# Performance work log

Measured on AMD Instinct MI355X. Metric: run time of the kernel, lower is better.

## Reference

```python
import jax, jax.numpy as jnp
import numpy as np

B, T, N, D = 8, 12, 325, 256
H = 8
HD = D // H
FF = 1024
SCALE = HD ** -0.5
EPS = 1e-5
NEG_INF = jnp.float32(-1e30)


def layernorm(x, w, b):
    mu = jnp.mean(x, axis=-1, keepdims=True)
    var = jnp.mean(jnp.square(x - mu), axis=-1, keepdims=True)
    return (x - mu) * jax.lax.rsqrt(var + EPS) * w + b


def mha(x, wq, bq, wk, bk, wv, bv, wo, bo, mask):
    # x: (G, L, D); mask: (L, L) bool, True = keep, or None
    G, L, _ = x.shape
    q = (x @ wq + bq).reshape(G, L, H, HD)
    k = (x @ wk + bk).reshape(G, L, H, HD)
    v = (x @ wv + bv).reshape(G, L, H, HD)
    scores = jnp.einsum('glhd,gmhd->ghlm', q, k) * SCALE
    if mask is not None:
        scores = jnp.where(mask[None, None], scores, NEG_INF)
    attn = jax.nn.softmax(scores, axis=-1)
    out = jnp.einsum('ghlm,gmhd->glhd', attn, v).reshape(G, L, D)
    return out @ wo + bo


def setup_inputs() -> dict:
    key = jax.random.key(0)
    ks = jax.random.split(key, 16)
    s = 0.02
    inp = {
        'x': jax.random.normal(ks[0], (B, T, N, D), jnp.float32),
        'adj_mask': jax.random.randint(ks[1], (N, N), 0, 2, jnp.int32),
        'sa_wq': jax.random.normal(ks[2], (D, D)) * s, 'sa_bq': jnp.zeros((D,)),
        'sa_wk': jax.random.normal(ks[3], (D, D)) * s, 'sa_bk': jnp.zeros((D,)),
        'sa_wv': jax.random.normal(ks[4], (D, D)) * s, 'sa_bv': jnp.zeros((D,)),
        'sa_wo': jax.random.normal(ks[5], (D, D)) * s, 'sa_bo': jnp.zeros((D,)),
        'sa_ln_w': jnp.ones((D,)), 'sa_ln_b': jnp.zeros((D,)),
        'ta_wq': jax.random.normal(ks[6], (D, D)) * s, 'ta_bq': jnp.zeros((D,)),
        'ta_wk': jax.random.normal(ks[7], (D, D)) * s, 'ta_bk': jnp.zeros((D,)),
        'ta_wv': jax.random.normal(ks[8], (D, D)) * s, 'ta_bv': jnp.zeros((D,)),
        'ta_wo': jax.random.normal(ks[9], (D, D)) * s, 'ta_bo': jnp.zeros((D,)),
        'ta_ln_w': jnp.ones((D,)), 'ta_ln_b': jnp.zeros((D,)),
        'f_w1': jax.random.normal(ks[10], (D, FF)) * s, 'f_b1': jnp.zeros((FF,)),
        'f_w2': jax.random.normal(ks[11], (FF, D)) * s, 'f_b2': jnp.zeros((D,)),
        'f_ln_w': jnp.ones((D,)), 'f_ln_b': jnp.zeros((D,)),
    }
    return inp


def reference(x, adj_mask,
              sa_wq, sa_bq, sa_wk, sa_bk, sa_wv, sa_bv, sa_wo, sa_bo, sa_ln_w, sa_ln_b,
              ta_wq, ta_bq, ta_wk, ta_bk, ta_wv, ta_bv, ta_wo, ta_bo, ta_ln_w, ta_ln_b,
              f_w1, f_b1, f_w2, f_b2, f_ln_w, f_ln_b):
    # Spatial attention over N at each (b, t)
    xs = x.reshape(B * T, N, D)
    sa = mha(xs, sa_wq, sa_bq, sa_wk, sa_bk, sa_wv, sa_bv, sa_wo, sa_bo,
             adj_mask != 0).reshape(B, T, N, D)
    x = layernorm(x + sa, sa_ln_w, sa_ln_b)

    # Temporal attention over T at each (b, n), causal
    xt = x.transpose(0, 2, 1, 3).reshape(B * N, T, D)
    causal = jnp.tril(jnp.ones((T, T), dtype=bool))
    ta = mha(xt, ta_wq, ta_bq, ta_wk, ta_bk, ta_wv, ta_bv, ta_wo, ta_bo, causal)
    ta = ta.reshape(B, N, T, D).transpose(0, 2, 1, 3)
    x = layernorm(x + ta, ta_ln_w, ta_ln_b)

    # FFN with exact GELU (torch nn.GELU default)
    h = jax.nn.gelu(x @ f_w1 + f_b1, approximate=False)
    out = layernorm(x + (h @ f_w2 + f_b2), f_ln_w, f_ln_b)
    return out
```

## Files before the change

### kernel.cpp

```cpp
#include <hip/hip_runtime.h>
#include <hip/hip_bf16.h>
#include <math.h>

#define B_   8
#define T_   12
#define NN   325
#define DD   256
#define HH   8
#define HD   32
#define FFD  1024
#define MTOK (B_*T_*NN)
#define QKVD 768
#define ATT_SCALE 0.17677669529663687f
#define LN_EPS 1e-5f
#define MROWS 336

typedef __attribute__((ext_vector_type(8))) __bf16 bf16x8;
typedef __attribute__((ext_vector_type(4))) float  f32x4;
typedef __attribute__((ext_vector_type(4))) short  shortx4;
typedef __attribute__((ext_vector_type(8))) unsigned short ushortx8;

static __device__ inline float bf2f(unsigned short u) {
  union { float f; unsigned int i; } c; c.i = ((unsigned int)u) << 16; return c.f;
}

#if __has_builtin(__builtin_amdgcn_mfma_f32_16x16x16bf16_1k)
#define MFMA16(a,b,c) __builtin_amdgcn_mfma_f32_16x16x16bf16_1k((a),(b),(c),0,0,0)
#else
static __device__ inline f32x4 mfma16_fn(shortx4 a, shortx4 b, f32x4 c) {
  f32x4 d;
  asm volatile("v_mfma_f32_16x16x16_bf16 %0, %1, %2, %3"
               : "=v"(d) : "v"(a), "v"(b), "v"(c));
  return d;
}
#define MFMA16(a,b,c) mfma16_fn((a),(b),(c))
#endif

__global__ __launch_bounds__(256) void gemm_strip2(
    const __hip_bfloat16* __restrict__ A,
    const __hip_bfloat16* __restrict__ Wt,
    const float* __restrict__ bias,
    __hip_bfloat16* __restrict__ Cb,
    int Mr, int Nr, int Kr, int gelu)
{
  constexpr int BP = 136;
  __shared__ __hip_bfloat16 Bs[128 * BP];

  const int NS  = Nr >> 7;
  const int nwg = gridDim.x;
  const int orig = blockIdx.x;
  const int qq = nwg >> 3, rr = nwg & 7;
  const int xcd = orig & 7, off = orig >> 3;
  const int id = (xcd < rr ? xcd * (qq + 1) : rr * (qq + 1) + (xcd - rr) * qq) + off;
  const int n0 = (id % NS) * 128;
  const int mg = id / NS;

  const int tid = threadIdx.x;
  const int w = tid >> 6, lane = tid & 63;
  const int lr = lane & 15, lg = lane >> 4;
  const int KC = Kr >> 7;

  float bv[8];
  #pragma unroll
  for (int j = 0; j < 8; ++j) bv[j] = bias[n0 + j * 16 + lr];

  const int strip0 = mg * 128 + w * 32;
  int ar0 = strip0 + lr;      if (ar0 >= Mr) ar0 = Mr - 1;
  int ar1 = strip0 + 16 + lr; if (ar1 >= Mr) ar1 = Mr - 1;

  f32x4 acc0[8] = {}, acc1[8] = {};

  for (int kc = 0; kc < KC; ++kc) {
    if (kc) __syncthreads();
    for (int u = tid; u < 128 * 16; u += 256) {
      int row = u >> 4, c8 = (u & 15) * 8;
      *(bf16x8*)&Bs[row * BP + c8] =
          *(const bf16x8*)&Wt[(size_t)(n0 + row) * Kr + kc * 128 + c8];
    }
    __syncthreads();

    const __hip_bfloat16* a0p = A + (size_t)ar0 * Kr + kc * 128 + lg * 8;
    const __hip_bfloat16* a1p = A + (size_t)ar1 * Kr + kc * 128 + lg * 8;
    bf16x8 a0[4], a1[4];
    #pragma unroll
    for (int k = 0; k < 4; ++k) {
      a0[k] = *(const bf16x8*)(a0p + k * 32);
      a1[k] = *(const bf16x8*)(a1p + k * 32);
    }
    #pragma unroll
    for (int k = 0; k < 4; ++k)
      #pragma unroll
      for (int j = 0; j < 8; ++j) {
        bf16x8 bfr = *(const bf16x8*)&Bs[(j * 16 + lr) * BP + k * 32 + lg * 8];
        acc0[j] = __builtin_amdgcn_mfma_f32_16x16x32_bf16(a0[k], bfr, acc0[j], 0, 0, 0);
        acc1[j] = __builtin_amdgcn_mfma_f32_16x16x32_bf16(a1[k], bfr, acc1[j], 0, 0, 0);
      }
  }

  #pragma unroll
  for (int j = 0; j < 8; ++j) {
    int col = n0 + j * 16 + lr;
    #pragma unroll
    for (int q = 0; q < 4; ++q) {
      int g0 = strip0 + lg * 4 + q;
      if (g0 < Mr) {
        float c = acc0[j][q] + bv[j];
        if (gelu) c = 0.5f * c * (1.f + erff(c * 0.70710678118654752f));
        Cb[(size_t)g0 * Nr + col] = __float2bfloat16(c);
      }
      int g1 = strip0 + 16 + lg * 4 + q;
      if (g1 < Mr) {
        float c = acc1[j][q] + bv[j];
        if (gelu) c = 0.5f * c * (1.f + erff(c * 0.70710678118654752f));
        Cb[(size_t)g1 * Nr + col] = __float2bfloat16(c);
      }
    }
  }
}

struct PrepPtrs {
  const float* w[10];
  const float* b[6];
};

__global__ __launch_bounds__(256) void prep_all(
    PrepPtrs p, const int* __restrict__ adj, const float* __restrict__ x0,
    __hip_bfloat16* __restrict__ Wb, float* __restrict__ qkvb,
    float* __restrict__ maskf, __hip_bfloat16* __restrict__ x0b)
{
  __shared__ float t[32][33];
  const int z = blockIdx.z;

  if (z < 10) {
    const int Kz = (z == 9) ? 1024 : 256;
    const int Nz = (z == 8) ? 1024 : 256;
    if ((int)blockIdx.x >= Nz / 32 || (int)blockIdx.y >= Kz / 32) return;
    static const unsigned int dsto[10] = {0, 65536, 131072, 196608, 262144,
                                          327680, 393216, 458752, 524288, 786432};
    const float scale = (z == 0 || z == 3) ? ATT_SCALE : 1.f;
    const float* W = p.w[z];
    __hip_bfloat16* Wt = Wb + dsto[z];
    const int n0 = blockIdx.x * 32, k0 = blockIdx.y * 32;
    const int tx = threadIdx.x & 31, ty = threadIdx.x >> 5;
    #pragma unroll
    for (int i = 0; i < 32; i += 8)
      t[ty + i][tx] = W[(size_t)(k0 + ty + i) * Nz + n0 + tx];
    __syncthreads();
    #pragma unroll
    for (int i = 0; i < 32; i += 8)
      Wt[(size_t)(n0 + ty + i) * Kz + k0 + tx] = __float2bfloat16(t[tx][ty + i] * scale);
    return;
  }

  const int bx = blockIdx.x + blockIdx.y * 32;
  const int gid = bx * 256 + threadIdx.x;

  if (z == 10) {
    if (gid < 1536) {
      int i = gid & 767;
      int which = gid < 768 ? 0 : 1;
      int sub = i >> 8, j = i & 255;
      float v = p.b[which * 3 + sub][j];
      if (sub == 0) v *= ATT_SCALE;
      qkvb[which * 768 + i] = v;
    } else if (gid < 1536 + NN * MROWS) {
      int idx = gid - 1536;
      int l = idx / MROWS, m = idx % MROWS;
      float v;
      if (m >= NN) v = -INFINITY;
      else v = (adj[l * NN + m] != 0) ? 0.f : -1e30f;
      maskf[idx] = v;
    }
    return;
  }

  const int n4 = MTOK * DD / 4;
  for (int i = gid; i < n4; i += 262144) {
    float4 v = reinterpret_cast<const float4*>(x0)[i];
    union { shortx4 s; __hip_bfloat16 h[4]; } u;
    u.h[0] = __float2bfloat16(v.x); u.h[1] = __float2bfloat16(v.y);
    u.h[2] = __float2bfloat16(v.z); u.h[3] = __float2bfloat16(v.w);
    reinterpret_cast<shortx4*>(x0b)[i] = u.s;
  }
}

__global__ __launch_bounds__(256) void spatial_attn_mfma(
    const __hip_bfloat16* __restrict__ qkv,
    const float* __restrict__ maskf,
    __hip_bfloat16* __restrict__ out)
{
  constexpr int KP = 40;
  constexpr int VP = 340;
  __shared__ unsigned short Kl[MROWS * KP];
  __shared__ unsigned short Vt[32 * VP];

  const int g = blockIdx.x, h = blockIdx.y;
  const int tid = threadIdx.x;
  const int w = tid >> 6, lane = tid & 63;
  const int lq = lane & 15, lg = lane >> 4;

  const size_t baseQ = (size_t)g * NN * QKVD + (size_t)h * HD;
  const size_t baseK = baseQ + 256;
  const size_t baseV = baseQ + 512;

  for (int idx = tid; idx < 32 * (VP - NN); idx += 256) {
    int d = idx / (VP - NN), kk = NN + idx % (VP - NN);
    Vt[d * VP + kk] = 0;
  }
  for (int idx = tid; idx < (MROWS - NN) * KP; idx += 256)
    Kl[NN * KP + idx] = 0;
  for (int idx = tid; idx < NN * 4; idx += 256) {
    int row = idx >> 2, cc = (idx & 3) * 8;
    union { bf16x8 v; unsigned short u[8]; } kv, vv;
    kv.v = *(const bf16x8*)&qkv[baseK + (size_t)row * QKVD + cc];
    *(bf16x8*)&Kl[row * KP + cc] = kv.v;
    vv.v = *(const bf16x8*)&qkv[baseV + (size_t)row * QKVD + cc];
    #pragma unroll
    for (int j = 0; j < 8; ++j) Vt[(cc + j) * VP + row] = vv.u[j];
  }
  __syncthreads();

  for (int qt = w; qt < 21; qt += 4) {
    const int query = qt * 16 + lq;
    const int qc = query < NN ? query : NN - 1;
    const bf16x8 qf = *(const bf16x8*)&qkv[baseQ + (size_t)qc * QKVD + lg * 8];
    const float* mrow = maskf + (size_t)qc * MROWS;

    f32x4 accL = {0.f, 0.f, 0.f, 0.f};
    f32x4 accH = {0.f, 0.f, 0.f, 0.f};
    float mrun = -INFINITY, lrun = 0.f;

    for (int t = 0; t < 21; ++t) {
      const int kbase = t * 16 + lg * 4;
      bf16x8 kf = *(const bf16x8*)&Kl[(t * 16 + lq) * KP + lg * 8];
      f32x4 st = __builtin_amdgcn_mfma_f32_16x16x32_bf16(
          kf, qf, (f32x4){0.f, 0.f, 0.f, 0.f}, 0, 0, 0);
      float4 mb = *(const float4*)&mrow[kbase];
      float s0 = st[0] + mb.x, s1 = st[1] + mb.y;
      float s2 = st[2] + mb.z, s3 = st[3] + mb.w;

      float tmax = fmaxf(fmaxf(s0, s1), fmaxf(s2, s3));
      tmax = fmaxf(tmax, __shfl_xor(tmax, 16));
      tmax = fmaxf(tmax, __shfl_xor(tmax, 32));
      const float mnew = fmaxf(mrun, tmax);
      const float corr = __expf(mrun - mnew);
      mrun = mnew;

      float p0 = __expf(s0 - mnew), p1 = __expf(s1 - mnew);
      float p2 = __expf(s2 - mnew), p3 = __expf(s3 - mnew);
      lrun = lrun * corr + ((p0 + p1) + (p2 + p3));
      accL *= corr; accH *= corr;

      union { shortx4 s4; __hip_bfloat16 hh[4]; } up;
      up.hh[0] = __float2bfloat16(p0); up.hh[1] = __float2bfloat16(p1);
      up.hh[2] = __float2bfloat16(p2); up.hh[3] = __float2bfloat16(p3);
      shortx4 vaL = *(const shortx4*)&Vt[lq * VP + kbase];
      shortx4 vaH = *(const shortx4*)&Vt[(lq + 16) * VP + kbase];
      accL = MFMA16(vaL, up.s4, accL);
      accH = MFMA16(vaH, up.s4, accH);
    }

    lrun += __shfl_xor(lrun, 16);
    lrun += __shfl_xor(lrun, 32);

    if (query < NN) {
      const float inv = 1.f / lrun;
      const size_t ob = ((size_t)(g * NN + query)) * DD + (size_t)h * HD;
      union { shortx4 s4; __hip_bfloat16 hh[4]; } uL, uH;
      #pragma unroll
      for (int q = 0; q < 4; ++q) {
        uL.hh[q] = __float2bfloat16(accL[q] * inv);
        uH.hh[q] = __float2bfloat16(accH[q] * inv);
      }
      *(shortx4*)&out[ob + lg * 4]      = uL.s4;
      *(shortx4*)&out[ob + 16 + lg * 4] = uH.s4;
    }
  }
}

__global__ __launch_bounds__(256) void temporal_attn(
    const __hip_bfloat16* __restrict__ qkv, __hip_bfloat16* __restrict__ out)
{
  int idx = blockIdx.x * 256 + threadIdx.x;
  const int total = B_ * NN * HH * T_;
  if (idx >= total) return;

  int t  = idx % T_;
  int h  = (idx / T_) % HH;
  int n  = (idx / (T_ * HH)) % NN;
  int b  = idx / (T_ * HH * NN);

  const size_t tq = (size_t)((b * T_ + t) * NN + n) * QKVD + h * HD;
  float qr[HD];
  #pragma unroll
  for (int c8 = 0; c8 < 4; ++c8) {
    ushortx8 u = *(const ushortx8*)&qkv[tq + c8 * 8];
    #pragma unroll
    for (int j = 0; j < 8; ++j) qr[c8 * 8 + j] = bf2f(u[j]);
  }

  float o[HD] = {};
  float mrun = -INFINITY, lrun = 0.f;

  for (int tt = 0; tt <= t; ++tt) {
    const size_t tk = (size_t)((b * T_ + tt) * NN + n) * QKVD + h * HD;
    float s = 0.f;
    #pragma unroll
    for (int c8 = 0; c8 < 4; ++c8) {
      ushortx8 u = *(const ushortx8*)&qkv[tk + 256 + c8 * 8];
      #pragma unroll
      for (int j = 0; j < 8; ++j) s += qr[c8 * 8 + j] * bf2f(u[j]);
    }
    float mnew = fmaxf(mrun, s);
    float corr = __expf(mrun - mnew);
    float p = __expf(s - mnew);
    lrun = lrun * corr + p;
    #pragma unroll
    for (int c8 = 0; c8 < 4; ++c8) {
      ushortx8 u = *(const ushortx8*)&qkv[tk + 512 + c8 * 8];
      #pragma unroll
      for (int j = 0; j < 8; ++j) o[c8 * 8 + j] = o[c8 * 8 + j] * corr + p * bf2f(u[j]);
    }
    mrun = mnew;
  }

  float inv = 1.f / lrun;
  __hip_bfloat16* op = out + ((size_t)((b * T_ + t) * NN + n)) * DD + h * HD;
  #pragma unroll
  for (int d0 = 0; d0 < HD; d0 += 4) {
    union { shortx4 s; __hip_bfloat16 h4[4]; } u;
    #pragma unroll
    for (int j = 0; j < 4; ++j) u.h4[j] = __float2bfloat16(o[d0 + j] * inv);
    *reinterpret_cast<shortx4*>(op + d0) = u.s;
  }
}

__global__ __launch_bounds__(64) void add_ln(
    const float* __restrict__ x, const __hip_bfloat16* __restrict__ r,
    const float* __restrict__ w, const float* __restrict__ bb,
    float* __restrict__ y, __hip_bfloat16* __restrict__ ybf)
{
  const size_t row = blockIdx.x;
  const int lane = threadIdx.x;

  const float4 xv = reinterpret_cast<const float4*>(x + row * DD)[lane];
  union { shortx4 s4; unsigned short u[4]; } rv;
  rv.s4 = reinterpret_cast<const shortx4*>(r + row * DD)[lane];
  float e[4] = {xv.x + bf2f(rv.u[0]), xv.y + bf2f(rv.u[1]),
                xv.z + bf2f(rv.u[2]), xv.w + bf2f(rv.u[3])};

  float s  = e[0] + e[1] + e[2] + e[3];
  float ss = e[0]*e[0] + e[1]*e[1] + e[2]*e[2] + e[3]*e[3];
  #pragma unroll
  for (int off = 32; off > 0; off >>= 1) {
    s  += __shfl_xor(s,  off, 64);
    ss += __shfl_xor(ss, off, 64);
  }
  float mu  = s * (1.f / DD);
  float var = ss * (1.f / DD) - mu * mu;
  float rs  = rsqrtf(var + LN_EPS);

  const float4 wv = reinterpret_cast<const float4*>(w)[lane];
  const float4 bv = reinterpret_cast<const float4*>(bb)[lane];
  float o0 = (e[0] - mu) * rs * wv.x + bv.x;
  float o1 = (e[1] - mu) * rs * wv.y + bv.y;
  float o2 = (e[2] - mu) * rs * wv.z + bv.z;
  float o3 = (e[3] - mu) * rs * wv.w + bv.w;
  float4 yv = {o0, o1, o2, o3};
  reinterpret_cast<float4*>(y + row * DD)[lane] = yv;
  if (ybf) {
    union { shortx4 s4; __hip_bfloat16 h4[4]; } u;
    u.h4[0] = __float2bfloat16(o0); u.h4[1] = __float2bfloat16(o1);
    u.h4[2] = __float2bfloat16(o2); u.h4[3] = __float2bfloat16(o3);
    reinterpret_cast<shortx4*>(ybf + row * DD)[lane] = u.s4;
  }
}

extern "C" void kernel_launch(void* const* d_in, const int* in_sizes, int n_in,
                              void* d_out, int out_size, void* d_ws, size_t ws_size,
                              hipStream_t stream)
{
  const float* x0   = (const float*)d_in[0];
  const int*   adj  = (const int*)  d_in[1];
  const float* sa_wq = (const float*)d_in[2];
  const float* sa_bq = (const float*)d_in[3];
  const float* sa_wk = (const float*)d_in[4];
  const float* sa_bk = (const float*)d_in[5];
  const float* sa_wv = (const float*)d_in[6];
  const float* sa_bv = (const float*)d_in[7];
  const float* sa_wo = (const float*)d_in[8];
  const float* sa_bo = (const float*)d_in[9];
  const float* sa_lw = (const float*)d_in[10];
  const float* sa_lb = (const float*)d_in[11];
  const float* ta_wq = (const float*)d_in[12];
  const float* ta_bq = (const float*)d_in[13];
  const float* ta_wk = (const float*)d_in[14];
  const float* ta_bk = (const float*)d_in[15];
  const float* ta_wv = (const float*)d_in[16];
  const float* ta_bv = (const float*)d_in[17];
  const float* ta_wo = (const float*)d_in[18];
  const float* ta_bo = (const float*)d_in[19];
  const float* ta_lw = (const float*)d_in[20];
  const float* ta_lb = (const float*)d_in[21];
  const float* f_w1  = (const float*)d_in[22];
  const float* f_b1  = (const float*)d_in[23];
  const float* f_w2  = (const float*)d_in[24];
  const float* f_b2  = (const float*)d_in[25];
  const float* f_lw  = (const float*)d_in[26];
  const float* f_lb  = (const float*)d_in[27];

  float* out = (float*)d_out;
  float* ws  = (float*)d_ws;

  const size_t P = (size_t)MTOK * DD;
  if (ws_size < 7 * P * sizeof(float)) return;

  float* R0 = ws;
  __hip_bfloat16* QKVb = (__hip_bfloat16*)(ws + P);
  __hip_bfloat16* HIDb = (__hip_bfloat16*)(ws + P);
  __hip_bfloat16* PRJ  = (__hip_bfloat16*)(ws + 3 * P);
  float* R4 = ws + 4 * P;
  __hip_bfloat16* X0b  = (__hip_bfloat16*)(ws + 5 * P);
  __hip_bfloat16* X1b  = (__hip_bfloat16*)(ws + 5 * P + P / 2);
  __hip_bfloat16* ATTb = (__hip_bfloat16*)(ws + 6 * P);
  __hip_bfloat16* Wb   = (__hip_bfloat16*)(ws + 6 * P + P / 2);

  __hip_bfloat16* sa_qkv_t = Wb;
  __hip_bfloat16* ta_qkv_t = Wb + 196608;
  __hip_bfloat16* sa_wo_t  = Wb + 393216;
  __hip_bfloat16* ta_wo_t  = Wb + 458752;
  __hip_bfloat16* f_w1_t   = Wb + 524288;
  __hip_bfloat16* f_w2_t   = Wb + 786432;
  float* qkvb  = (float*)(Wb + 1048576);
  float* maskf = qkvb + 1536;

  PrepPtrs pp;
  pp.w[0] = sa_wq; pp.w[1] = sa_wk; pp.w[2] = sa_wv;
  pp.w[3] = ta_wq; pp.w[4] = ta_wk; pp.w[5] = ta_wv;
  pp.w[6] = sa_wo; pp.w[7] = ta_wo; pp.w[8] = f_w1; pp.w[9] = f_w2;
  pp.b[0] = sa_bq; pp.b[1] = sa_bk; pp.b[2] = sa_bv;
  pp.b[3] = ta_bq; pp.b[4] = ta_bk; pp.b[5] = ta_bv;
  prep_all<<<dim3(32, 32, 12), 256, 0, stream>>>(pp, adj, x0, Wb, qkvb, maskf, X0b);

  const int MG = (MTOK + 127) / 128;
  auto gemmS = [&](const __hip_bfloat16* A, const __hip_bfloat16* Wt, const float* bias,
                   __hip_bfloat16* Cb, int Nr, int Kr, int gelu) {
    int nwg = (Nr / 128) * MG;
    gemm_strip2<<<nwg, 256, 0, stream>>>(A, Wt, bias, Cb, MTOK, Nr, Kr, gelu);
  };

  gemmS(X0b, sa_qkv_t, qkvb, QKVb, QKVD, DD, 0);
  spatial_attn_mfma<<<dim3(B_ * T_, HH), 256, 0, stream>>>(QKVb, maskf, ATTb);
  gemmS(ATTb, sa_wo_t, sa_bo, PRJ, DD, DD, 0);
  add_ln<<<MTOK, 64, 0, stream>>>(x0, PRJ, sa_lw, sa_lb, R4, X1b);

  gemmS(X1b, ta_qkv_t, qkvb + 768, QKVb, QKVD, DD, 0);
  {
    int total = B_ * NN * HH * T_;
    temporal_attn<<<(total + 255) / 256, 256, 0, stream>>>(QKVb, ATTb);
  }
  gemmS(ATTb, ta_wo_t, ta_bo, PRJ, DD, DD, 0);
  add_ln<<<MTOK, 64, 0, stream>>>(R4, PRJ, ta_lw, ta_lb, R0, X0b);

  gemmS(X0b, f_w1_t, f_b1, HIDb, FFD, DD, 1);
  gemmS(HIDb, f_w2_t, f_b2, PRJ, DD, FFD, 0);
  add_ln<<<MTOK, 64, 0, stream>>>(R0, PRJ, f_lw, f_lb, out, nullptr);
}
```

Baseline: 345.1 us.

## Fuse FFN up-projection, GELU and down-projection into one kernel

Replaces the two FFN GEMM launches with a single kernel in which each wave holds 16 tokens, computes 64-wide hidden chunks with MFMA, applies bias and exact GELU in registers, and feeds them straight into the second GEMM's accumulators. This avoids writing and re-reading the 31200x1024 bf16 hidden tensor through global memory. The catch is that every block streams the full W1 and W2 weights straight from global or cache with no LDS staging, and each thread holds 16 accumulator tiles, which may raise register pressure and lower occupancy.

```diff
diff --git a/kernel.cpp b/kernel.cpp
--- a/kernel.cpp
+++ b/kernel.cpp
@@ -114,6 +114,85 @@
         if (gelu) c = 0.5f * c * (1.f + erff(c * 0.70710678118654752f));
         Cb[(size_t)g1 * Nr + col] = __float2bfloat16(c);
       }
+    }
+  }
+}
+
+__global__ __launch_bounds__(256) void ffn_fused(
+    const __hip_bfloat16* __restrict__ X,
+    const __hip_bfloat16* __restrict__ W1t,
+    const float* __restrict__ b1,
+    const __hip_bfloat16* __restrict__ W2t,
+    const float* __restrict__ b2,
+    __hip_bfloat16* __restrict__ Cb,
+    int Mr)
+{
+  const int tid = threadIdx.x;
+  const int w = tid >> 6, lane = tid & 63;
+  const int lr = lane & 15, lg = lane >> 4;
+
+  const int tok = blockIdx.x * 64 + w * 16 + lr;
+  const int tc  = tok < Mr ? tok : Mr - 1;
+
+  bf16x8 af[8];
+  #pragma unroll
+  for (int ks = 0; ks < 8; ++ks)
+    af[ks] = *(const bf16x8*)&X[(size_t)tc * DD + ks * 32 + lg * 8];
+
+  f32x4 acc[16] = {};
+
+  #pragma unroll 1
+  for (int hc = 0; hc < 16; ++hc) {
+    const int h0 = hc * 64;
+
+    f32x4 ht[4] = {};
+    #pragma unroll
+    for (int j = 0; j < 4; ++j) {
+      const __hip_bfloat16* w1p = W1t + (size_t)(h0 + j * 16 + lr) * DD + lg * 8;
+      #pragma unroll
+      for (int ks = 0; ks < 8; ++ks) {
+        bf16x8 w1f = *(const bf16x8*)(w1p + ks * 32);
+        ht[j] = __builtin_amdgcn_mfma_f32_16x16x32_bf16(w1f, af[ks], ht[j], 0, 0, 0);
+      }
+    }
+
+    shortx4 hb[4];
+    #pragma unroll
+    for (int j = 0; j < 4; ++j) {
+      float4 bj = *(const float4*)&b1[h0 + j * 16 + lg * 4];
+      const float b4[4] = {bj.x, bj.y, bj.z, bj.w};
+      union { shortx4 s4; __hip_bfloat16 hh[4]; } u;
+      #pragma unroll
+      for (int q = 0; q < 4; ++q) {
+        float v = ht[j][q] + b4[q];
+        v = 0.5f * v * (1.f + erff(v * 0.70710678118654752f));
+        u.hh[q] = __float2bfloat16(v);
+      }
+      hb[j] = u.s4;
+    }
+
+    #pragma unroll
+    for (int jd = 0; jd < 16; ++jd) {
+      const __hip_bfloat16* w2p = W2t + (size_t)(jd * 16 + lr) * FFD + h0 + lg * 4;
+      #pragma unroll
+      for (int j = 0; j < 4; ++j) {
+        shortx4 w2f = *(const shortx4*)(w2p + j * 16);
+        acc[jd] = MFMA16(w2f, hb[j], acc[jd]);
+      }
+    }
+  }
+
+  if (tok < Mr) {
+    #pragma unroll
+    for (int jd = 0; jd < 16; ++jd) {
+      const int col = jd * 16 + lg * 4;
+      float4 bj = *(const float4*)&b2[col];
+      const float b4[4] = {bj.x, bj.y, bj.z, bj.w};
+      union { shortx4 s4; __hip_bfloat16 hh[4]; } u;
+      #pragma unroll
+      for (int q = 0; q < 4; ++q)
+        u.hh[q] = __float2bfloat16(acc[jd][q] + b4[q]);
+      *(shortx4*)&Cb[(size_t)tok * DD + col] = u.s4;
     }
   }
 }
@@ -417,7 +496,6 @@
 
   float* R0 = ws;
   __hip_bfloat16* QKVb = (__hip_bfloat16*)(ws + P);
-  __hip_bfloat16* HIDb = (__hip_bfloat16*)(ws + P);
   __hip_bfloat16* PRJ  = (__hip_bfloat16*)(ws + 3 * P);
   float* R4 = ws + 4 * P;
   __hip_bfloat16* X0b  = (__hip_bfloat16*)(ws + 5 * P);
@@ -462,7 +540,7 @@
   gemmS(ATTb, ta_wo_t, ta_bo, PRJ, DD, DD, 0);
   add_ln<<<MTOK, 64, 0, stream>>>(R4, PRJ, ta_lw, ta_lb, R0, X0b);
 
-  gemmS(X0b, f_w1_t, f_b1, HIDb, FFD, DD, 1);
-  gemmS(HIDb, f_w2_t, f_b2, PRJ, DD, FFD, 0);
+  ffn_fused<<<(MTOK + 63) / 64, 256, 0, stream>>>(
+      X0b, f_w1_t, f_b1, f_w2_t, f_b2, PRJ, MTOK);
   add_ln<<<MTOK, 64, 0, stream>>>(R0, PRJ, f_lw, f_lb, out, nullptr);
 }
```

New measurement: 606.5 us. 1.76x slower.
